# Performance work log

Measured on AMD Instinct MI355X. Metric: run time of the kernel, lower is better.

Reference implementation:

```python
import jax, jax.numpy as jnp
import numpy as np

B, H, W, D = 64, 56, 56, 128
WS = 7            # window size per axis
NH = 4            # attention heads
L = 2             # transformer layers (layer 1 is shifted)
HID = 4 * D
G1, G2 = H // WS, W // WS
G, N = G1 * G2, WS * WS
SH = WS // 2      # cyclic shift


def _build_attn_mask():
    # faithful port of ShiftWindow mask construction (numpy constants)
    img = np.zeros((H, W), dtype=np.float32)
    sl = (slice(0, -WS), slice(-WS, -SH), slice(-SH, None))
    idx = 0
    for s0 in sl:
        for s1 in sl:
            img[s0, s1] = idx
            idx += 1
    win = img.reshape(G1, WS, G2, WS).transpose(0, 2, 1, 3).reshape(G, N)
    diff = win[:, None, :] - win[:, :, None]          # [G, N, N]
    return jnp.asarray(np.where(diff != 0, -100.0, 0.0).astype(np.float32))

ATTN_MASK = _build_attn_mask()


def setup_inputs() -> dict:
    key = jax.random.key(0)
    ks = jax.random.split(key, 8)
    s = 0.02
    return {
        'x': jax.random.normal(ks[0], (B, H, W, D), jnp.float32),
        'ln1_g': jnp.ones((L, D)), 'ln1_b': jnp.zeros((L, D)),
        'qkv_w': s * jax.random.normal(ks[1], (L, D, 3 * D)), 'qkv_b': jnp.zeros((L, 3 * D)),
        'proj_w': s * jax.random.normal(ks[2], (L, D, D)), 'proj_b': jnp.zeros((L, D)),
        'ln2_g': jnp.ones((L, D)), 'ln2_b': jnp.zeros((L, D)),
        'mlp_w1': s * jax.random.normal(ks[3], (L, D, HID)), 'mlp_b1': jnp.zeros((L, HID)),
        'mlp_w2': s * jax.random.normal(ks[4], (L, HID, D)), 'mlp_b2': jnp.zeros((L, D)),
        'ds_norm_g': jnp.ones((4 * D,)), 'ds_norm_b': jnp.zeros((4 * D,)),
        'ds_w': s * jax.random.normal(ks[5], (4 * D, 2 * D)),
    }


def _ln(x, g, b, eps=1e-5):
    m = jnp.mean(x, -1, keepdims=True)
    v = jnp.mean((x - m) ** 2, -1, keepdims=True)
    return (x - m) * jax.lax.rsqrt(v + eps) * g + b


def _partition(x):
    # [B, H, W, D] -> [B, G, N, D]
    x = x.reshape(B, G1, WS, G2, WS, D).transpose(0, 1, 3, 2, 4, 5)
    return x.reshape(B, G, N, D)


def _unpartition(xw):
    x = xw.reshape(B, G1, G2, WS, WS, D).transpose(0, 1, 3, 2, 4, 5)
    return x.reshape(B, H, W, D)


def _block(xw, mask, i, p):
    # pre-norm window attention
    h = _ln(xw, p['ln1_g'][i], p['ln1_b'][i])
    qkv = h @ p['qkv_w'][i] + p['qkv_b'][i]                 # [B,G,N,3D]
    q, k, v = jnp.split(qkv, 3, axis=-1)
    hd = D // NH
    q = q.reshape(B, G, N, NH, hd)
    k = k.reshape(B, G, N, NH, hd)
    v = v.reshape(B, G, N, NH, hd)
    scores = jnp.einsum('bgnhd,bgmhd->bghnm', q, k) / jnp.sqrt(jnp.float32(hd))
    if mask is not None:
        scores = scores + mask[None, :, None, :, :]         # [1,G,1,N,N]
    attn = jax.nn.softmax(scores, axis=-1)
    o = jnp.einsum('bghnm,bgmhd->bgnhd', attn, v).reshape(B, G, N, D)
    xw = xw + o @ p['proj_w'][i] + p['proj_b'][i]
    # MLP
    h = _ln(xw, p['ln2_g'][i], p['ln2_b'][i])
    h = jax.nn.gelu(h @ p['mlp_w1'][i] + p['mlp_b1'][i])
    return xw + h @ p['mlp_w2'][i] + p['mlp_b2'][i]


def reference(x, ln1_g, ln1_b, qkv_w, qkv_b, proj_w, proj_b, ln2_g, ln2_b,
              mlp_w1, mlp_b1, mlp_w2, mlp_b2, ds_norm_g, ds_norm_b, ds_w):
    p = dict(ln1_g=ln1_g, ln1_b=ln1_b, qkv_w=qkv_w, qkv_b=qkv_b,
             proj_w=proj_w, proj_b=proj_b, ln2_g=ln2_g, ln2_b=ln2_b,
             mlp_w1=mlp_w1, mlp_b1=mlp_b1, mlp_w2=mlp_w2, mlp_b2=mlp_b2)
    xw = _partition(x)
    for i in range(L):
        shift = (i % 2 == 1)
        if shift:
            xw = _partition(jnp.roll(_unpartition(xw), (-SH, -SH), axis=(1, 2)))
            xw = _block(xw, ATTN_MASK, i, p)
            xw = _partition(jnp.roll(_unpartition(xw), (SH, SH), axis=(1, 2)))
        else:
            xw = _block(xw, None, i, p)
    x = _unpartition(xw)
    # Downsample: 2x2 patch merge -> LN -> Linear(4D -> 2D) (no bias)
    x = x.reshape(B, H // 2, 2, W // 2, 2, D).transpose(0, 1, 3, 2, 4, 5)
    x = x.reshape(B, H // 2, W // 2, 4 * D)
    x = _ln(x, ds_norm_g, ds_norm_b) @ ds_w
    return x
```

## Files before the change

### kernel.cpp

```cpp
#include <hip/hip_runtime.h>
#include <hip/hip_bf16.h>


typedef short bf16x8 __attribute__((ext_vector_type(8)));
typedef float f32x4 __attribute__((ext_vector_type(4)));
typedef unsigned short u16;
typedef unsigned int u32;

#define MTOK 200704
#define DSTOK 50176

__device__ __forceinline__ u16 f2b(float f){
  u32 u = __float_as_uint(f);
  u += 0x7fffu + ((u >> 16) & 1u);
  return (u16)(u >> 16);
}
__device__ __forceinline__ float blo(u32 u){ return __uint_as_float(u << 16); }
__device__ __forceinline__ float bhi(u32 u){ return __uint_as_float(u & 0xffff0000u); }

__device__ __forceinline__ float gelu_tanh(float v){
  float u = 0.7978845608028654f * (v + 0.044715f * v * v * v);
  u = fminf(u, 10.f);
  float e = __expf(2.f * u);
  float t = (e - 1.f) / (e + 1.f);
  return 0.5f * v * (1.f + t);
}

__global__ void transpose_cvt(const float* __restrict__ src, u16* __restrict__ dst,
                              int K, int N){
  int e = blockIdx.x * 256 + threadIdx.x;
  if (e >= K * N) return;
  int k = e / N, n = e - k * N;
  dst[n * K + k] = f2b(src[e]);
}

template<int MODE>
__global__ __launch_bounds__(256) void ln_kernel(const float* __restrict__ src,
    const float* __restrict__ gw, const float* __restrict__ bw,
    u16* __restrict__ dst)
{
  int wv = threadIdx.x >> 6, lane = threadIdx.x & 63;
  int t = blockIdx.x * 4 + wv;
  long soff;
  if (MODE == 2) {
    soff = (long)t * 128;
  } else {
    int n = t % 49; int tq = t / 49; int gg = tq & 63; int b_ = tq >> 6;
    int r = n / 7, c = n - 7 * r;
    int h = (gg >> 3) * 7 + r, w = (gg & 7) * 7 + c;
    if (MODE == 1) { h += 3; if (h >= 56) h -= 56; w += 3; if (w >= 56) w -= 56; }
    soff = ((long)((b_ * 56 + h) * 56 + w)) * 128;
  }
  float2 v = *(const float2*)(src + soff + lane * 2);
  float s = v.x + v.y, s2 = v.x * v.x + v.y * v.y;
  #pragma unroll
  for (int o = 32; o; o >>= 1) { s += __shfl_xor(s, o); s2 += __shfl_xor(s2, o); }
  float mean = s * 0.0078125f;
  float var  = s2 * 0.0078125f - mean * mean;
  float rstd = rsqrtf(var + 1e-5f);
  int c0 = lane * 2;
  ushort2 o2;
  o2.x = f2b((v.x - mean) * rstd * gw[c0]   + bw[c0]);
  o2.y = f2b((v.y - mean) * rstd * gw[c0+1] + bw[c0+1]);
  *(ushort2*)(dst + (long)t * 128 + c0) = o2;
}

__global__ __launch_bounds__(256) void ds_ln_kernel(const float* __restrict__ x,
    const float* __restrict__ gw, const float* __restrict__ bw,
    u16* __restrict__ dst)
{
  int wv = threadIdx.x >> 6, lane = threadIdx.x & 63;
  int t = blockIdx.x * 4 + wv;
  int j = t % 28; int tq = t / 28; int i = tq % 28; int b_ = tq / 28;
  int e0 = lane * 8;
  int p = e0 >> 8, q = (e0 >> 7) & 1, d = e0 & 127;
  const float* src = x + ((long)((b_ * 56 + 2*i + p) * 56 + 2*j + q)) * 128 + d;
  float4 a  = *(const float4*)src;
  float4 b4 = *(const float4*)(src + 4);
  float vs[8] = {a.x, a.y, a.z, a.w, b4.x, b4.y, b4.z, b4.w};
  float s = 0.f, s2 = 0.f;
  #pragma unroll
  for (int u = 0; u < 8; u++) { s += vs[u]; s2 += vs[u] * vs[u]; }
  #pragma unroll
  for (int o = 32; o; o >>= 1) { s += __shfl_xor(s, o); s2 += __shfl_xor(s2, o); }
  float mean = s * (1.f / 512.f);
  float var  = s2 * (1.f / 512.f) - mean * mean;
  float rstd = rsqrtf(var + 1e-5f);
  u16 ov[8];
  #pragma unroll
  for (int u = 0; u < 8; u++) ov[u] = f2b((vs[u] - mean) * rstd * gw[e0+u] + bw[e0+u]);
  uint4 o4;
  o4.x = (u32)ov[0] | ((u32)ov[1] << 16);
  o4.y = (u32)ov[2] | ((u32)ov[3] << 16);
  o4.z = (u32)ov[4] | ((u32)ov[5] << 16);
  o4.w = (u32)ov[6] | ((u32)ov[7] << 16);
  *(uint4*)(dst + (long)t * 512 + e0) = o4;
}

template<int MASKED>
__global__ __launch_bounds__(256) void attn_mfma(const u16* __restrict__ qkv,
                                                 u16* __restrict__ obuf)
{
  __shared__ u16 Pls_all[4][64][72];
  const int h = threadIdx.x >> 6;
  const int lane = threadIdx.x & 63;
  const int c = lane & 15, g = lane >> 4;
  const int wi = blockIdx.x;
  const int g_ = wi & 63;
  const long t0 = (long)wi * 49;
  u16 (*Pls)[72] = Pls_all[h];

  bf16x8 qf[4], kf[4];
  #pragma unroll
  for (int mi = 0; mi < 4; mi++) {
    int r = 16*mi + c; r = r > 48 ? 48 : r;
    qf[mi] = *(const bf16x8*)(qkv + (t0 + r)*384 + h*32 + g*8);
  }
  #pragma unroll
  for (int ni = 0; ni < 4; ni++) {
    int r = 16*ni + c; r = r > 48 ? 48 : r;
    kf[ni] = *(const bf16x8*)(qkv + (t0 + r)*384 + 128 + h*32 + g*8);
  }

  f32x4 acc[4][4];
  const f32x4 zero4 = {0.f, 0.f, 0.f, 0.f};
  #pragma unroll
  for (int mi = 0; mi < 4; mi++)
    #pragma unroll
    for (int ni = 0; ni < 4; ni++)
      acc[mi][ni] = __builtin_amdgcn_mfma_f32_16x16x32_bf16(qf[mi], kf[ni], zero4, 0, 0, 0);

  bf16x8 vf[2][2];
  #pragma unroll
  for (int ni2 = 0; ni2 < 2; ni2++)
    #pragma unroll
    for (int ks = 0; ks < 2; ks++)
      #pragma unroll
      for (int jj = 0; jj < 8; jj++) {
        int k = ks*32 + 8*g + jj; k = k > 48 ? 48 : k;
        vf[ni2][ks][jj] = (short)qkv[(t0 + k)*384 + 256 + h*32 + 16*ni2 + c];
      }

  int rid_c[4];
  int g1b = 0, g2b = 0;
  if (MASKED) {
    g1b = (g_ >> 3) * 7; g2b = (g_ & 7) * 7;
    #pragma unroll
    for (int ni = 0; ni < 4; ni++) {
      int col = 16*ni + c; col = col > 48 ? 48 : col;
      int cr = col / 7, cc = col - 7*cr;
      int hh = g1b + cr, ww = g2b + cc;
      rid_c[ni] = (hh < 49 ? 0 : (hh < 53 ? 1 : 2)) * 3 + (ww < 49 ? 0 : (ww < 53 ? 1 : 2));
    }
  }

  #pragma unroll
  for (int mi = 0; mi < 4; mi++) {
    #pragma unroll
    for (int j = 0; j < 4; j++) {
      int rr = 16*mi + 4*g + j;
      int rid_r = 0;
      if (MASKED) {
        int r2 = rr > 48 ? 48 : rr;
        int rh = r2 / 7, rw = r2 - 7*rh;
        int hh = g1b + rh, ww = g2b + rw;
        rid_r = (hh < 49 ? 0 : (hh < 53 ? 1 : 2)) * 3 + (ww < 49 ? 0 : (ww < 53 ? 1 : 2));
      }
      float sv[4];
      #pragma unroll
      for (int ni = 0; ni < 4; ni++) {
        float s = acc[mi][ni][j] * 0.17677669529663687f;
        int col = 16*ni + c;
        if (col >= 49) s = -1e30f;
        else if (MASKED && rid_c[ni] != rid_r) s -= 100.f;
        sv[ni] = s;
      }
      float m4 = fmaxf(fmaxf(sv[0], sv[1]), fmaxf(sv[2], sv[3]));
      #pragma unroll
      for (int o = 1; o <= 8; o <<= 1) m4 = fmaxf(m4, __shfl_xor(m4, o));
      float p[4], sum = 0.f;
      #pragma unroll
      for (int ni = 0; ni < 4; ni++) { p[ni] = __expf(sv[ni] - m4); sum += p[ni]; }
      #pragma unroll
      for (int o = 1; o <= 8; o <<= 1) sum += __shfl_xor(sum, o);
      float rs = 1.f / sum;
      #pragma unroll
      for (int ni = 0; ni < 4; ni++)
        Pls[rr][16*ni + c] = f2b(p[ni] * rs);
    }
  }

  __syncthreads();

  f32x4 accO[4][2];
  #pragma unroll
  for (int mi = 0; mi < 4; mi++)
    #pragma unroll
    for (int ni2 = 0; ni2 < 2; ni2++) accO[mi][ni2] = zero4;
  #pragma unroll
  for (int mi = 0; mi < 4; mi++)
    #pragma unroll
    for (int ks = 0; ks < 2; ks++) {
      bf16x8 pa = *(const bf16x8*)(&Pls[16*mi + c][ks*32 + g*8]);
      #pragma unroll
      for (int ni2 = 0; ni2 < 2; ni2++)
        accO[mi][ni2] = __builtin_amdgcn_mfma_f32_16x16x32_bf16(pa, vf[ni2][ks], accO[mi][ni2], 0, 0, 0);
    }

  #pragma unroll
  for (int mi = 0; mi < 4; mi++)
    #pragma unroll
    for (int ni2 = 0; ni2 < 2; ni2++)
      #pragma unroll
      for (int j = 0; j < 4; j++) {
        int r = 16*mi + 4*g + j;
        if (r < 49)
          obuf[(t0 + r)*128 + h*32 + 16*ni2 + c] = f2b(accO[mi][ni2][j]);
      }
}

template<int K, int EPI>
__global__ __launch_bounds__(256) void gemm_kernel(
    const u16* __restrict__ A, const u16* __restrict__ Bt,
    const float* __restrict__ bias, int Ntot,
    u16* __restrict__ outb, float* __restrict__ outf,
    const float* __restrict__ resbase, int shift)
{
  __shared__ __align__(16) u16 sh[16384];
  u16* Asl = sh;
  u16* Bsl = sh + 8192;
  float (*Cf)[128] = (float(*)[128])sh;

  const int tid = threadIdx.x;
  const int row0 = blockIdx.x * 128, col0 = blockIdx.y * 128;
  const int wv = tid >> 6, lane = tid & 63;
  const int m_off = (wv >> 1) * 64, n_off = (wv & 1) * 64;
  const int lr = lane & 15, lk = (lane >> 4) * 8;

  f32x4 acc[4][4];
  const f32x4 zero4 = {0.f, 0.f, 0.f, 0.f};
  #pragma unroll
  for (int a1 = 0; a1 < 4; a1++)
    #pragma unroll
    for (int a2 = 0; a2 < 4; a2++) acc[a1][a2] = zero4;

  for (int k0 = 0; k0 < K; k0 += 64) {
    __syncthreads();
    #pragma unroll
    for (int j = 0; j < 4; j++) {
      int ch = tid + j * 256;
      int r = ch >> 3, cc = ch & 7;
      int col = k0 + ((cc * 8) ^ ((r & 7) << 3));
      __builtin_amdgcn_global_load_lds(
          (const __attribute__((address_space(1))) u32*)(A + (long)(row0 + r) * K + col),
          (__attribute__((address_space(3))) u32*)(Asl + ch * 8), 16, 0, 0);
      __builtin_amdgcn_global_load_lds(
          (const __attribute__((address_space(1))) u32*)(Bt + (long)(col0 + r) * K + col),
          (__attribute__((address_space(3))) u32*)(Bsl + ch * 8), 16, 0, 0);
    }
    __syncthreads();
    #pragma unroll
    for (int kk = 0; kk < 64; kk += 32) {
      bf16x8 af[4], bfr[4];
      #pragma unroll
      for (int mi = 0; mi < 4; mi++) {
        int R = m_off + mi*16 + lr;
        af[mi] = *(const bf16x8*)&Asl[R*64 + ((kk + lk) ^ ((R & 7) << 3))];
      }
      #pragma unroll
      for (int ni = 0; ni < 4; ni++) {
        int R = n_off + ni*16 + lr;
        bfr[ni] = *(const bf16x8*)&Bsl[R*64 + ((kk + lk) ^ ((R & 7) << 3))];
      }
      #pragma unroll
      for (int mi = 0; mi < 4; mi++)
        #pragma unroll
        for (int ni = 0; ni < 4; ni++)
          acc[mi][ni] = __builtin_amdgcn_mfma_f32_16x16x32_bf16(
              af[mi], bfr[ni], acc[mi][ni], 0, 0, 0);
    }
  }

  const int g = lane >> 4;
  #pragma unroll
  for (int half = 0; half < 2; half++) {
    __syncthreads();
    if ((wv >> 1) == half) {
      #pragma unroll
      for (int mi = 0; mi < 4; mi++)
        #pragma unroll
        for (int ni = 0; ni < 4; ni++)
          #pragma unroll
          for (int j = 0; j < 4; j++) {
            int lrow = mi*16 + 4*g + j;
            int col  = n_off + ni*16 + lr;
            Cf[lrow][col ^ ((lrow & 7) << 2)] = acc[mi][ni][j];
          }
    }
    __syncthreads();
    #pragma unroll
    for (int jj = 0; jj < 8; jj++) {
      int ch = tid + jj * 256;
      int r = ch >> 5, c4 = ch & 31;
      float4 v = *(const float4*)&Cf[r][(c4*4) ^ ((r & 7) << 2)];
      int grow = row0 + half*64 + r;
      int gcol = col0 + c4*4;
      if (EPI == 0 || EPI == 1) {
        float4 b4 = *(const float4*)&bias[gcol];
        float v0 = v.x + b4.x, v1 = v.y + b4.y, v2 = v.z + b4.z, v3 = v.w + b4.w;
        if (EPI == 1) { v0 = gelu_tanh(v0); v1 = gelu_tanh(v1); v2 = gelu_tanh(v2); v3 = gelu_tanh(v3); }
        uint2 o2;
        o2.x = (u32)f2b(v0) | ((u32)f2b(v1) << 16);
        o2.y = (u32)f2b(v2) | ((u32)f2b(v3) << 16);
        *(uint2*)(outb + (long)grow * Ntot + gcol) = o2;
      } else if (EPI == 2) {
        float4 b4 = *(const float4*)&bias[gcol];
        int n = grow % 49; int tq = grow / 49; int gg = tq & 63; int b_ = tq >> 6;
        int rr = n / 7, cc = n - 7 * rr;
        int hh = (gg >> 3) * 7 + rr, ww = (gg & 7) * 7 + cc;
        if (shift) { hh += 3; if (hh >= 56) hh -= 56; ww += 3; if (ww >= 56) ww -= 56; }
        long obase = ((long)((b_ * 56 + hh) * 56 + ww)) * 128;
        float4 res = *(const float4*)&resbase[obase + gcol];
        float4 o;
        o.x = res.x + v.x + b4.x; o.y = res.y + v.y + b4.y;
        o.z = res.z + v.z + b4.z; o.w = res.w + v.w + b4.w;
        *(float4*)&outf[obase + gcol] = o;
      } else if (EPI == 3) {
        float4 b4 = *(const float4*)&bias[gcol];
        float4 cur = *(const float4*)&outf[(long)grow * 128 + gcol];
        cur.x += v.x + b4.x; cur.y += v.y + b4.y;
        cur.z += v.z + b4.z; cur.w += v.w + b4.w;
        *(float4*)&outf[(long)grow * 128 + gcol] = cur;
      } else {
        *(float4*)&outf[(long)grow * Ntot + gcol] = v;
      }
    }
  }
}

extern "C" void kernel_launch(void* const* d_in, const int* in_sizes, int n_in,
                              void* d_out, int out_size, void* d_ws, size_t ws_size,
                              hipStream_t stream)
{
  const float* x_in   = (const float*)d_in[0];
  const float* ln1_g  = (const float*)d_in[1];
  const float* ln1_b  = (const float*)d_in[2];
  const float* qkv_w  = (const float*)d_in[3];
  const float* qkv_b  = (const float*)d_in[4];
  const float* proj_w = (const float*)d_in[5];
  const float* proj_b = (const float*)d_in[6];
  const float* ln2_g  = (const float*)d_in[7];
  const float* ln2_b  = (const float*)d_in[8];
  const float* w1     = (const float*)d_in[9];
  const float* b1     = (const float*)d_in[10];
  const float* w2     = (const float*)d_in[11];
  const float* b2     = (const float*)d_in[12];
  const float* dsg    = (const float*)d_in[13];
  const float* dsb    = (const float*)d_in[14];
  const float* dsw    = (const float*)d_in[15];

  float* x_ws   = (float*)d_ws;
  u16* buf_h    = (u16*)(x_ws + (long)MTOK * 128);
  u16* buf_o    = buf_h;
  u16* buf_big  = buf_h + (long)MTOK * 128;
  u16* wts      = buf_big + (long)MTOK * 512;
  u16* qkv_wt   = wts;
  u16* proj_wt  = qkv_wt  + 2 * 49152;
  u16* w1t      = proj_wt + 2 * 16384;
  u16* w2t      = w1t     + 2 * 65536;
  u16* ds_wt    = w2t     + 2 * 65536;

  for (int i = 0; i < 2; i++) {
    transpose_cvt<<<(49152+255)/256, 256, 0, stream>>>(qkv_w  + i*49152, qkv_wt  + i*49152, 128, 384);
    transpose_cvt<<<(16384+255)/256, 256, 0, stream>>>(proj_w + i*16384, proj_wt + i*16384, 128, 128);
    transpose_cvt<<<(65536+255)/256, 256, 0, stream>>>(w1     + i*65536, w1t     + i*65536, 128, 512);
    transpose_cvt<<<(65536+255)/256, 256, 0, stream>>>(w2     + i*65536, w2t     + i*65536, 512, 128);
  }
  transpose_cvt<<<(131072+255)/256, 256, 0, stream>>>(dsw, ds_wt, 512, 256);

  for (int i = 0; i < 2; i++) {
    if (i == 0) ln_kernel<0><<<MTOK/4, 256, 0, stream>>>(x_in, ln1_g,       ln1_b,       buf_h);
    else        ln_kernel<1><<<MTOK/4, 256, 0, stream>>>(x_ws, ln1_g + 128, ln1_b + 128, buf_h);
    gemm_kernel<128,0><<<dim3(MTOK/128, 3), 256, 0, stream>>>(
        buf_h, qkv_wt + i*49152, qkv_b + i*384, 384, buf_big, nullptr, nullptr, 0);
    if (i == 0) attn_mfma<0><<<4096, 256, 0, stream>>>(buf_big, buf_o);
    else        attn_mfma<1><<<4096, 256, 0, stream>>>(buf_big, buf_o);
    gemm_kernel<128,2><<<dim3(MTOK/128, 1), 256, 0, stream>>>(
        buf_o, proj_wt + i*16384, proj_b + i*128, 128, nullptr, x_ws,
        (i == 0 ? x_in : (const float*)x_ws), i);
    ln_kernel<2><<<MTOK/4, 256, 0, stream>>>(x_ws, ln2_g + i*128, ln2_b + i*128, buf_h);
    gemm_kernel<128,1><<<dim3(MTOK/128, 4), 256, 0, stream>>>(
        buf_h, w1t + i*65536, b1 + i*512, 512, buf_big, nullptr, nullptr, 0);
    gemm_kernel<512,3><<<dim3(MTOK/128, 1), 256, 0, stream>>>(
        buf_big, w2t + i*65536, b2 + i*128, 128, nullptr, x_ws, x_ws, 0);
  }

  ds_ln_kernel<<<DSTOK/4, 256, 0, stream>>>(x_ws, dsg, dsb, buf_h);
  gemm_kernel<512,4><<<dim3(DSTOK/128, 2), 256, 0, stream>>>(
      buf_h, ds_wt, nullptr, 256, nullptr, (float*)d_out, nullptr, 0);
}
```

Measured before the change: 1.183 ms.

## Fuse MLP into one kernel, fold LayerNorms into epilogues, store residual as bf16

Adds a fused MLP kernel that keeps the 128x512 GELU hidden activations in shared memory in 128-column chunks, so the large intermediate never goes through global memory. LayerNorm 2 moves into the projection GEMM epilogue, and the next layer's LN1 with its shifted window partition moves into the MLP epilogue, which drops separate LN kernels. The residual stream is stored in bf16 rather than fp32 to halve its traffic. The cost is lower residual precision and a fused kernel with more shared memory and registers, which may lower occupancy.

After: 1.227 ms. 3.7% more time.

```diff
diff --git a/kernel.cpp b/kernel.cpp
--- a/kernel.cpp
+++ b/kernel.cpp
@@ -17,6 +17,7 @@
 }
 __device__ __forceinline__ float blo(u32 u){ return __uint_as_float(u << 16); }
 __device__ __forceinline__ float bhi(u32 u){ return __uint_as_float(u & 0xffff0000u); }
+__device__ __forceinline__ float b2f(u16 u){ return __uint_as_float(((u32)u) << 16); }
 
 __device__ __forceinline__ float gelu_tanh(float v){
   float u = 0.7978845608028654f * (v + 0.044715f * v * v * v);
@@ -26,6 +27,10 @@
   return 0.5f * v * (1.f + t);
 }
 
+#define GLDS(gp, lp) __builtin_amdgcn_global_load_lds( \
+    (const __attribute__((address_space(1))) u32*)(gp), \
+    (__attribute__((address_space(3))) u32*)(lp), 16, 0, 0)
+
 __global__ void transpose_cvt(const float* __restrict__ src, u16* __restrict__ dst,
                               int K, int N){
   int e = blockIdx.x * 256 + threadIdx.x;
@@ -34,23 +39,16 @@
   dst[n * K + k] = f2b(src[e]);
 }
 
-template<int MODE>
-__global__ __launch_bounds__(256) void ln_kernel(const float* __restrict__ src,
+__global__ __launch_bounds__(256) void ln0_kernel(const float* __restrict__ src,
     const float* __restrict__ gw, const float* __restrict__ bw,
     u16* __restrict__ dst)
 {
   int wv = threadIdx.x >> 6, lane = threadIdx.x & 63;
   int t = blockIdx.x * 4 + wv;
-  long soff;
-  if (MODE == 2) {
-    soff = (long)t * 128;
-  } else {
-    int n = t % 49; int tq = t / 49; int gg = tq & 63; int b_ = tq >> 6;
-    int r = n / 7, c = n - 7 * r;
-    int h = (gg >> 3) * 7 + r, w = (gg & 7) * 7 + c;
-    if (MODE == 1) { h += 3; if (h >= 56) h -= 56; w += 3; if (w >= 56) w -= 56; }
-    soff = ((long)((b_ * 56 + h) * 56 + w)) * 128;
-  }
+  int n = t % 49; int tq = t / 49; int gg = tq & 63; int b_ = tq >> 6;
+  int r = n / 7, c = n - 7 * r;
+  int h = (gg >> 3) * 7 + r, w = (gg & 7) * 7 + c;
+  long soff = ((long)((b_ * 56 + h) * 56 + w)) * 128;
   float2 v = *(const float2*)(src + soff + lane * 2);
   float s = v.x + v.y, s2 = v.x * v.x + v.y * v.y;
   #pragma unroll
@@ -65,7 +63,7 @@
   *(ushort2*)(dst + (long)t * 128 + c0) = o2;
 }
 
-__global__ __launch_bounds__(256) void ds_ln_kernel(const float* __restrict__ x,
+__global__ __launch_bounds__(256) void ds_ln_kernel(const u16* __restrict__ x,
     const float* __restrict__ gw, const float* __restrict__ bw,
     u16* __restrict__ dst)
 {
@@ -74,10 +72,10 @@
   int j = t % 28; int tq = t / 28; int i = tq % 28; int b_ = tq / 28;
   int e0 = lane * 8;
   int p = e0 >> 8, q = (e0 >> 7) & 1, d = e0 & 127;
-  const float* src = x + ((long)((b_ * 56 + 2*i + p) * 56 + 2*j + q)) * 128 + d;
-  float4 a  = *(const float4*)src;
-  float4 b4 = *(const float4*)(src + 4);
-  float vs[8] = {a.x, a.y, a.z, a.w, b4.x, b4.y, b4.z, b4.w};
+  const u16* src = x + ((long)((b_ * 56 + 2*i + p) * 56 + 2*j + q)) * 128 + d;
+  uint4 a = *(const uint4*)src;
+  float vs[8] = {blo(a.x), bhi(a.x), blo(a.y), bhi(a.y),
+                 blo(a.z), bhi(a.z), blo(a.w), bhi(a.w)};
   float s = 0.f, s2 = 0.f;
   #pragma unroll
   for (int u = 0; u < 8; u++) { s += vs[u]; s2 += vs[u] * vs[u]; }
@@ -219,12 +217,14 @@
       }
 }
 
-template<int K, int EPI>
+template<int K, int EPI, int RESF32>
 __global__ __launch_bounds__(256) void gemm_kernel(
     const u16* __restrict__ A, const u16* __restrict__ Bt,
     const float* __restrict__ bias, int Ntot,
     u16* __restrict__ outb, float* __restrict__ outf,
-    const float* __restrict__ resbase, int shift)
+    u16* __restrict__ outx, const float* __restrict__ resf, int shift,
+    const float* __restrict__ lng, const float* __restrict__ lnb,
+    u16* __restrict__ lnout)
 {
   __shared__ __align__(16) u16 sh[16384];
   u16* Asl = sh;
@@ -251,12 +251,8 @@
       int ch = tid + j * 256;
       int r = ch >> 3, cc = ch & 7;
       int col = k0 + ((cc * 8) ^ ((r & 7) << 3));
-      __builtin_amdgcn_global_load_lds(
-          (const __attribute__((address_space(1))) u32*)(A + (long)(row0 + r) * K + col),
-          (__attribute__((address_space(3))) u32*)(Asl + ch * 8), 16, 0, 0);
-      __builtin_amdgcn_global_load_lds(
-          (const __attribute__((address_space(1))) u32*)(Bt + (long)(col0 + r) * K + col),
-          (__attribute__((address_space(3))) u32*)(Bsl + ch * 8), 16, 0, 0);
+      GLDS(A  + (long)(row0 + r) * K + col, Asl + ch * 8);
+      GLDS(Bt + (long)(col0 + r) * K + col, Bsl + ch * 8);
     }
     __syncthreads();
     #pragma unroll
@@ -305,34 +301,214 @@
       float4 v = *(const float4*)&Cf[r][(c4*4) ^ ((r & 7) << 2)];
       int grow = row0 + half*64 + r;
       int gcol = col0 + c4*4;
-      if (EPI == 0 || EPI == 1) {
+      if (EPI == 0) {
         float4 b4 = *(const float4*)&bias[gcol];
-        float v0 = v.x + b4.x, v1 = v.y + b4.y, v2 = v.z + b4.z, v3 = v.w + b4.w;
-        if (EPI == 1) { v0 = gelu_tanh(v0); v1 = gelu_tanh(v1); v2 = gelu_tanh(v2); v3 = gelu_tanh(v3); }
         uint2 o2;
-        o2.x = (u32)f2b(v0) | ((u32)f2b(v1) << 16);
-        o2.y = (u32)f2b(v2) | ((u32)f2b(v3) << 16);
+        o2.x = (u32)f2b(v.x + b4.x) | ((u32)f2b(v.y + b4.y) << 16);
+        o2.y = (u32)f2b(v.z + b4.z) | ((u32)f2b(v.w + b4.w) << 16);
         *(uint2*)(outb + (long)grow * Ntot + gcol) = o2;
       } else if (EPI == 2) {
-        float4 b4 = *(const float4*)&bias[gcol];
         int n = grow % 49; int tq = grow / 49; int gg = tq & 63; int b_ = tq >> 6;
         int rr = n / 7, cc = n - 7 * rr;
         int hh = (gg >> 3) * 7 + rr, ww = (gg & 7) * 7 + cc;
         if (shift) { hh += 3; if (hh >= 56) hh -= 56; ww += 3; if (ww >= 56) ww -= 56; }
-        long obase = ((long)((b_ * 56 + hh) * 56 + ww)) * 128;
-        float4 res = *(const float4*)&resbase[obase + gcol];
-        float4 o;
-        o.x = res.x + v.x + b4.x; o.y = res.y + v.y + b4.y;
-        o.z = res.z + v.z + b4.z; o.w = res.w + v.w + b4.w;
-        *(float4*)&outf[obase + gcol] = o;
-      } else if (EPI == 3) {
+        long t = (long)(b_ * 56 + hh) * 56 + ww;
+        long obase = t * 128;
         float4 b4 = *(const float4*)&bias[gcol];
-        float4 cur = *(const float4*)&outf[(long)grow * 128 + gcol];
-        cur.x += v.x + b4.x; cur.y += v.y + b4.y;
-        cur.z += v.z + b4.z; cur.w += v.w + b4.w;
-        *(float4*)&outf[(long)grow * 128 + gcol] = cur;
+        float r0, r1, r2, r3;
+        if (RESF32) {
+          float4 res = *(const float4*)&resf[obase + gcol];
+          r0 = res.x; r1 = res.y; r2 = res.z; r3 = res.w;
+        } else {
+          uint2 cur = *(const uint2*)&outx[obase + gcol];
+          r0 = blo(cur.x); r1 = bhi(cur.x); r2 = blo(cur.y); r3 = bhi(cur.y);
+        }
+        float o0 = r0 + v.x + b4.x, o1 = r1 + v.y + b4.y;
+        float o2v = r2 + v.z + b4.z, o3 = r3 + v.w + b4.w;
+        uint2 xw;
+        xw.x = (u32)f2b(o0) | ((u32)f2b(o1) << 16);
+        xw.y = (u32)f2b(o2v) | ((u32)f2b(o3) << 16);
+        *(uint2*)(outx + obase + gcol) = xw;
+        float s = o0 + o1 + o2v + o3;
+        float s2 = o0*o0 + o1*o1 + o2v*o2v + o3*o3;
+        #pragma unroll
+        for (int o = 1; o <= 16; o <<= 1) { s += __shfl_xor(s, o); s2 += __shfl_xor(s2, o); }
+        float mean = s * 0.0078125f;
+        float var  = s2 * 0.0078125f - mean * mean;
+        float rstd = rsqrtf(var + 1e-5f);
+        float4 g4 = *(const float4*)&lng[gcol];
+        float4 bb4 = *(const float4*)&lnb[gcol];
+        uint2 lo2;
+        lo2.x = (u32)f2b((o0 - mean) * rstd * g4.x + bb4.x) |
+                ((u32)f2b((o1 - mean) * rstd * g4.y + bb4.y) << 16);
+        lo2.y = (u32)f2b((o2v - mean) * rstd * g4.z + bb4.z) |
+                ((u32)f2b((o3 - mean) * rstd * g4.w + bb4.w) << 16);
+        *(uint2*)(lnout + obase + gcol) = lo2;
       } else {
         *(float4*)&outf[(long)grow * Ntot + gcol] = v;
+      }
+    }
+  }
+}
+
+template<int WRITE_LN>
+__global__ __launch_bounds__(256) void mlp_kernel(
+    const u16* __restrict__ xh, const u16* __restrict__ w1t, const float* __restrict__ b1,
+    const u16* __restrict__ w2t, const float* __restrict__ b2,
+    u16* __restrict__ xrmw,
+    const float* __restrict__ lng, const float* __restrict__ lnb,
+    u16* __restrict__ lnout)
+{
+  __shared__ __align__(16) u16 S0[16384];
+  __shared__ __align__(16) u16 S1[16384];
+  const int tid = threadIdx.x;
+  const int row0 = blockIdx.x * 128;
+  const int wv = tid >> 6, lane = tid & 63;
+  const int m_off = (wv >> 1) * 64, n_off = (wv & 1) * 64;
+  const int lr = lane & 15, lk = (lane >> 4) * 8, g = lane >> 4;
+
+  f32x4 acc_o[4][4];
+  const f32x4 zero4 = {0.f, 0.f, 0.f, 0.f};
+  #pragma unroll
+  for (int a1 = 0; a1 < 4; a1++)
+    #pragma unroll
+    for (int a2 = 0; a2 < 4; a2++) acc_o[a1][a2] = zero4;
+
+  for (int nc = 0; nc < 4; nc++) {
+    __syncthreads();
+    #pragma unroll
+    for (int j = 0; j < 8; j++) {
+      int ch = tid + j * 256;
+      int r = ch >> 4, cc = ch & 15;
+      int col = (cc * 8) ^ ((r & 7) << 3);
+      GLDS(xh  + (long)(row0 + r) * 128 + col,      S0 + ch * 8);
+      GLDS(w1t + (long)(nc * 128 + r) * 128 + col,  S1 + ch * 8);
+    }
+    __syncthreads();
+    f32x4 acc_h[4][4];
+    #pragma unroll
+    for (int a1 = 0; a1 < 4; a1++)
+      #pragma unroll
+      for (int a2 = 0; a2 < 4; a2++) acc_h[a1][a2] = zero4;
+    #pragma unroll
+    for (int kk = 0; kk < 128; kk += 32) {
+      bf16x8 af[4], bfr[4];
+      #pragma unroll
+      for (int mi = 0; mi < 4; mi++) {
+        int R = m_off + mi*16 + lr;
+        af[mi] = *(const bf16x8*)&S0[R*128 + ((kk + lk) ^ ((R & 7) << 3))];
+      }
+      #pragma unroll
+      for (int ni = 0; ni < 4; ni++) {
+        int R = n_off + ni*16 + lr;
+        bfr[ni] = *(const bf16x8*)&S1[R*128 + ((kk + lk) ^ ((R & 7) << 3))];
+      }
+      #pragma unroll
+      for (int mi = 0; mi < 4; mi++)
+        #pragma unroll
+        for (int ni = 0; ni < 4; ni++)
+          acc_h[mi][ni] = __builtin_amdgcn_mfma_f32_16x16x32_bf16(
+              af[mi], bfr[ni], acc_h[mi][ni], 0, 0, 0);
+    }
+    __syncthreads();
+    #pragma unroll
+    for (int mi = 0; mi < 4; mi++)
+      #pragma unroll
+      for (int ni = 0; ni < 4; ni++)
+        #pragma unroll
+        for (int j = 0; j < 4; j++) {
+          int lrow = m_off + mi*16 + 4*g + j;
+          int col  = n_off + ni*16 + lr;
+          float hv = gelu_tanh(acc_h[mi][ni][j] + b1[nc*128 + col]);
+          S0[lrow*128 + (col ^ ((lrow & 7) << 3))] = f2b(hv);
+        }
+    #pragma unroll
+    for (int j = 0; j < 8; j++) {
+      int ch = tid + j * 256;
+      int r = ch >> 4, cc = ch & 15;
+      int col = (cc * 8) ^ ((r & 7) << 3);
+      GLDS(w2t + (long)r * 512 + nc * 128 + col, S1 + ch * 8);
+    }
+    __syncthreads();
+    #pragma unroll
+    for (int kk = 0; kk < 128; kk += 32) {
+      bf16x8 af[4], bfr[4];
+      #pragma unroll
+      for (int mi = 0; mi < 4; mi++) {
+        int R = m_off + mi*16 + lr;
+        af[mi] = *(const bf16x8*)&S0[R*128 + ((kk + lk) ^ ((R & 7) << 3))];
+      }
+      #pragma unroll
+      for (int ni = 0; ni < 4; ni++) {
+        int R = n_off + ni*16 + lr;
+        bfr[ni] = *(const bf16x8*)&S1[R*128 + ((kk + lk) ^ ((R & 7) << 3))];
+      }
+      #pragma unroll
+      for (int mi = 0; mi < 4; mi++)
+        #pragma unroll
+        for (int ni = 0; ni < 4; ni++)
+          acc_o[mi][ni] = __builtin_amdgcn_mfma_f32_16x16x32_bf16(
+              af[mi], bfr[ni], acc_o[mi][ni], 0, 0, 0);
+    }
+  }
+
+  float (*Cf)[128] = (float(*)[128])S0;
+  #pragma unroll
+  for (int half = 0; half < 2; half++) {
+    __syncthreads();
+    if ((wv >> 1) == half) {
+      #pragma unroll
+      for (int mi = 0; mi < 4; mi++)
+        #pragma unroll
+        for (int ni = 0; ni < 4; ni++)
+          #pragma unroll
+          for (int j = 0; j < 4; j++) {
+            int lrow = mi*16 + 4*g + j;
+            int col  = n_off + ni*16 + lr;
+            Cf[lrow][col ^ ((lrow & 7) << 2)] = acc_o[mi][ni][j];
+          }
+    }
+    __syncthreads();
+    #pragma unroll
+    for (int jj = 0; jj < 8; jj++) {
+      int ch = tid + jj * 256;
+      int r = ch >> 5, c4 = ch & 31;
+      float4 v = *(const float4*)&Cf[r][(c4*4) ^ ((r & 7) << 2)];
+      int t = row0 + half*64 + r;
+      int gcol = c4*4;
+      float4 b4 = *(const float4*)&b2[gcol];
+      uint2 cur = *(const uint2*)&xrmw[(long)t * 128 + gcol];
+      float o0 = blo(cur.x) + v.x + b4.x;
+      float o1 = bhi(cur.x) + v.y + b4.y;
+      float o2v = blo(cur.y) + v.z + b4.z;
+      float o3 = bhi(cur.y) + v.w + b4.w;
+      uint2 xw;
+      xw.x = (u32)f2b(o0) | ((u32)f2b(o1) << 16);
+      xw.y = (u32)f2b(o2v) | ((u32)f2b(o3) << 16);
+      *(uint2*)(xrmw + (long)t * 128 + gcol) = xw;
+      if (WRITE_LN) {
+        float s = o0 + o1 + o2v + o3;
+        float s2 = o0*o0 + o1*o1 + o2v*o2v + o3*o3;
+        #pragma unroll
+        for (int o = 1; o <= 16; o <<= 1) { s += __shfl_xor(s, o); s2 += __shfl_xor(s2, o); }
+        float mean = s * 0.0078125f;
+        float var  = s2 * 0.0078125f - mean * mean;
+        float rstd = rsqrtf(var + 1e-5f);
+        float4 g4  = *(const float4*)&lng[gcol];
+        float4 bb4 = *(const float4*)&lnb[gcol];
+        int b_ = t / 3136; int rem = t - b_ * 3136;
+        int hh = rem / 56, ww = rem - hh * 56;
+        int hs = hh + 53; if (hs >= 56) hs -= 56;
+        int ws = ww + 53; if (ws >= 56) ws -= 56;
+        int gg = (hs / 7) * 8 + (ws / 7);
+        int nn = (hs % 7) * 7 + (ws % 7);
+        long dst = ((long)(b_ * 64 + gg) * 49 + nn) * 128 + gcol;
+        uint2 lo2;
+        lo2.x = (u32)f2b((o0 - mean) * rstd * g4.x + bb4.x) |
+                ((u32)f2b((o1 - mean) * rstd * g4.y + bb4.y) << 16);
+        lo2.y = (u32)f2b((o2v - mean) * rstd * g4.z + bb4.z) |
+                ((u32)f2b((o3 - mean) * rstd * g4.w + bb4.w) << 16);
+        *(uint2*)(lnout + dst) = lo2;
       }
     }
   }
@@ -359,10 +535,10 @@
   const float* dsb    = (const float*)d_in[14];
   const float* dsw    = (const float*)d_in[15];
 
-  float* x_ws   = (float*)d_ws;
-  u16* buf_h    = (u16*)(x_ws + (long)MTOK * 128);
-  u16* buf_o    = buf_h;
-  u16* buf_big  = buf_h + (long)MTOK * 128;
+  u16* x_ws     = (u16*)d_ws;
+  u16* buf_h    = x_ws + (long)MTOK * 128;
+  u16* xh       = buf_h + (long)MTOK * 128;
+  u16* buf_big  = xh + (long)MTOK * 128;
   u16* wts      = buf_big + (long)MTOK * 512;
   u16* qkv_wt   = wts;
   u16* proj_wt  = qkv_wt  + 2 * 49152;
@@ -378,24 +554,30 @@
   }
   transpose_cvt<<<(131072+255)/256, 256, 0, stream>>>(dsw, ds_wt, 512, 256);
 
-  for (int i = 0; i < 2; i++) {
-    if (i == 0) ln_kernel<0><<<MTOK/4, 256, 0, stream>>>(x_in, ln1_g,       ln1_b,       buf_h);
-    else        ln_kernel<1><<<MTOK/4, 256, 0, stream>>>(x_ws, ln1_g + 128, ln1_b + 128, buf_h);
-    gemm_kernel<128,0><<<dim3(MTOK/128, 3), 256, 0, stream>>>(
-        buf_h, qkv_wt + i*49152, qkv_b + i*384, 384, buf_big, nullptr, nullptr, 0);
-    if (i == 0) attn_mfma<0><<<4096, 256, 0, stream>>>(buf_big, buf_o);
-    else        attn_mfma<1><<<4096, 256, 0, stream>>>(buf_big, buf_o);
-    gemm_kernel<128,2><<<dim3(MTOK/128, 1), 256, 0, stream>>>(
-        buf_o, proj_wt + i*16384, proj_b + i*128, 128, nullptr, x_ws,
-        (i == 0 ? x_in : (const float*)x_ws), i);
-    ln_kernel<2><<<MTOK/4, 256, 0, stream>>>(x_ws, ln2_g + i*128, ln2_b + i*128, buf_h);
-    gemm_kernel<128,1><<<dim3(MTOK/128, 4), 256, 0, stream>>>(
-        buf_h, w1t + i*65536, b1 + i*512, 512, buf_big, nullptr, nullptr, 0);
-    gemm_kernel<512,3><<<dim3(MTOK/128, 1), 256, 0, stream>>>(
-        buf_big, w2t + i*65536, b2 + i*128, 128, nullptr, x_ws, x_ws, 0);
-  }
-
-  ds_ln_kernel<<<DSTOK/4, 256, 0, stream>>>(x_ws, dsg, dsb, buf_h);
-  gemm_kernel<512,4><<<dim3(DSTOK/128, 2), 256, 0, stream>>>(
-      buf_h, ds_wt, nullptr, 256, nullptr, (float*)d_out, nullptr, 0);
-}
+  ln0_kernel<<<MTOK/4, 256, 0, stream>>>(x_in, ln1_g, ln1_b, buf_h);
+  gemm_kernel<128,0,0><<<dim3(MTOK/128, 3), 256, 0, stream>>>(
+      buf_h, qkv_wt, qkv_b, 384, buf_big, nullptr, nullptr, nullptr, 0,
+      nullptr, nullptr, nullptr);
+  attn_mfma<0><<<4096, 256, 0, stream>>>(buf_big, buf_h);
+  gemm_kernel<128,2,1><<<dim3(MTOK/128, 1), 256, 0, stream>>>(
+      buf_h, proj_wt, proj_b, 128, nullptr, nullptr, x_ws, x_in, 0,
+      ln2_g, ln2_b, xh);
+  mlp_kernel<1><<<MTOK/128, 256, 0, stream>>>(
+      xh, w1t, b1, w2t, b2, x_ws, ln1_g + 128, ln1_b + 128, buf_h);
+
+  gemm_kernel<128,0,0><<<dim3(MTOK/128, 3), 256, 0, stream>>>(
+      buf_h, qkv_wt + 49152, qkv_b + 384, 384, buf_big, nullptr, nullptr, nullptr, 0,
+      nullptr, nullptr, nullptr);
+  attn_mfma<1><<<4096, 256, 0, stream>>>(buf_big, buf_h);
+  gemm_kernel<128,2,0><<<dim3(MTOK/128, 1), 256, 0, stream>>>(
+      buf_h, proj_wt + 16384, proj_b + 128, 128, nullptr, nullptr, x_ws, nullptr, 1,
+      ln2_g + 128, ln2_b + 128, xh);
+  mlp_kernel<0><<<MTOK/128, 256, 0, stream>>>(
+      xh, w1t + 65536, b1 + 512, w2t + 65536, b2 + 128, x_ws,
+      nullptr, nullptr, nullptr);
+
+  ds_ln_kernel<<<DSTOK/4, 256, 0, stream>>>(x_ws, dsg, dsb, buf_big);
+  gemm_kernel<512,4,0><<<dim3(DSTOK/128, 2), 256, 0, stream>>>(
+      buf_big, ds_wt, nullptr, 256, nullptr, (float*)d_out, nullptr, nullptr, 0,
+      nullptr, nullptr, nullptr);
+}
```
